# Performance work log

Hardware: AMD Instinct MI355X
Metric: run time of the kernel (lower is better)

Reference implementation:

```python
import jax, jax.numpy as jnp
import numpy as np

INPUT_SIZE = 9 * 7 * 32  # 2016
HIDDEN = 100
NUM_CLASSES = 3


def setup_inputs() -> dict:
    key = jax.random.key(0)
    ks = jax.random.split(key, 7)
    B, T = 256, 256
    s_ih = 1.0 / np.sqrt(HIDDEN)
    x = jax.random.normal(ks[0], (B, T, INPUT_SIZE), dtype=jnp.float32)
    # PyTorch LSTM params: gate order (i, f, g, o), each block of size HIDDEN
    W_ih = jax.random.uniform(ks[1], (4 * HIDDEN, INPUT_SIZE), jnp.float32, -s_ih, s_ih)
    W_hh = jax.random.uniform(ks[2], (4 * HIDDEN, HIDDEN), jnp.float32, -s_ih, s_ih)
    b_ih = jax.random.uniform(ks[3], (4 * HIDDEN,), jnp.float32, -s_ih, s_ih)
    b_hh = jax.random.uniform(ks[4], (4 * HIDDEN,), jnp.float32, -s_ih, s_ih)
    s_fc = 1.0 / np.sqrt(HIDDEN)
    W_fc = jax.random.uniform(ks[5], (NUM_CLASSES, HIDDEN), jnp.float32, -s_fc, s_fc)
    b_fc = jax.random.uniform(ks[6], (NUM_CLASSES,), jnp.float32, -s_fc, s_fc)
    return {"x": x, "W_ih": W_ih, "W_hh": W_hh, "b_ih": b_ih, "b_hh": b_hh,
            "W_fc": W_fc, "b_fc": b_fc}


def _lstm_last_hidden(x, W_ih, W_hh, b_ih, b_hh):
    B, T, _ = x.shape
    H = W_hh.shape[1]
    # Precompute input projection for all timesteps as one big GEMM: [B,T,4H]
    x_proj = jnp.einsum('bti,gi->btg', x, W_ih) + (b_ih + b_hh)
    x_proj = jnp.swapaxes(x_proj, 0, 1)  # [T, B, 4H] for scan over time

    def step(carry, xp_t):
        h, c = carry
        gates = xp_t + h @ W_hh.T  # [B, 4H]
        i, f, g, o = jnp.split(gates, 4, axis=-1)
        i = jax.nn.sigmoid(i)
        f = jax.nn.sigmoid(f)
        g = jnp.tanh(g)
        o = jax.nn.sigmoid(o)
        c = f * c + i * g
        h = o * jnp.tanh(c)
        return (h, c), None

    h0 = jnp.zeros((B, H), dtype=x.dtype)
    c0 = jnp.zeros((B, H), dtype=x.dtype)
    (hT, _), _ = jax.lax.scan(step, (h0, c0), x_proj)
    return hT  # [B, H] == out[:, -1, :]


def reference(x, W_ih, W_hh, b_ih, b_hh, W_fc, b_fc):
    hT = _lstm_last_hidden(x, W_ih, W_hh, b_ih, b_hh)
    return hT @ W_fc.T + b_fc  # [B, 3]
```

## Files before the change

### kernel.cpp

```cpp
#include <hip/hip_runtime.h>
#include <cstdint>
#include <cstddef>

#define DINL __device__ __forceinline__

typedef float f32x4 __attribute__((ext_vector_type(4)));
typedef unsigned short u16x8 __attribute__((ext_vector_type(8)));
typedef __bf16 bf16x8 __attribute__((ext_vector_type(8)));
typedef _Float16 half2v __attribute__((ext_vector_type(2)));

static constexpr int I_SZ  = 2016;
static constexpr int G4H   = 400;
static constexpr int HID   = 100;
static constexpr int BATCH = 256;
static constexpr int TLEN  = 256;
static constexpr int MROWS = BATCH * TLEN;
static constexpr int KT    = 63;
static constexpr int NPAD  = 512;
static constexpr int LD    = 40;

DINL unsigned short f2bf(float f) {
  unsigned u = __float_as_uint(f);
  u += 0x7fffu + ((u >> 16) & 1u);
  return (unsigned short)(u >> 16);
}
DINL float bf2f(unsigned short v) { return __uint_as_float(((unsigned)v) << 16); }

DINL void async16(const unsigned short* g, unsigned short* l) {
  __builtin_amdgcn_global_load_lds(
      (const __attribute__((address_space(1))) unsigned int*)g,
      (__attribute__((address_space(3))) unsigned int*)l, 16, 0, 0);
}

#if __has_builtin(__builtin_amdgcn_fdot2)
DINL float fdot2f(half2v a, half2v b, float c) { return __builtin_amdgcn_fdot2(a, b, c, false); }
#else
DINL float fdot2f(half2v a, half2v b, float c) {
  return c + (float)a[0] * (float)b[0] + (float)a[1] * (float)b[1];
}
#endif

#if __has_builtin(__builtin_amdgcn_exp2f)
DINL float ex2(float x) { return __builtin_amdgcn_exp2f(x); }
#else
DINL float ex2(float x) { return exp2f(x); }
#endif
#if __has_builtin(__builtin_amdgcn_rcpf)
DINL float rcpf_(float x) { return __builtin_amdgcn_rcpf(x); }
#else
DINL float rcpf_(float x) { return 1.0f / x; }
#endif

DINL float fast_sigmoid(float x) { return rcpf_(1.0f + ex2(-1.44269504f * x)); }
DINL float fast_tanh(float x)    { return 1.0f - 2.0f * rcpf_(1.0f + ex2(2.88539008f * x)); }

DINL half2v bch2(unsigned v) { return __builtin_bit_cast(half2v, v); }

__global__ void prep_kernel(const float* __restrict__ W_ih,
                            const float* __restrict__ b_ih,
                            const float* __restrict__ b_hh,
                            unsigned short* __restrict__ Wb,
                            float* __restrict__ biasb) {
  int idx = blockIdx.x * 256 + threadIdx.x;
  const int total = KT * NPAD * LD;
  if (idx < total) {
    int kt = idx / (NPAD * LD);
    int r  = idx - kt * (NPAD * LD);
    int n  = r / LD;
    int kk = r - n * LD;
    unsigned short v = 0;
    if (n < G4H && kk < 32) v = f2bf(W_ih[n * I_SZ + kt * 32 + kk]);
    Wb[idx] = v;
  }
  if (idx < NPAD) biasb[idx] = (idx < G4H) ? (b_ih[idx] + b_hh[idx]) : 0.0f;
}

__global__ __launch_bounds__(512) void gemm_xproj(
    const float* __restrict__ x, const unsigned short* __restrict__ Wb,
    const float* __restrict__ biasb, unsigned short* __restrict__ xp) {
  __shared__ unsigned short Ab[2][128 * LD];
  __shared__ unsigned short Bb[2][NPAD * LD];

  const int tid  = threadIdx.x;
  const int lane = tid & 63;
  const int wv   = tid >> 6;
  const int wm   = wv & 3;
  const int wn   = wv >> 2;
  const int m0   = blockIdx.x * 128;
  const int arow = tid >> 2;
  const int akq  = tid & 3;
  const int l15  = lane & 15;
  const int l4   = lane >> 4;

  f32x4 acc[2][13];
#pragma unroll
  for (int i = 0; i < 2; ++i)
#pragma unroll
    for (int j = 0; j < 13; ++j) acc[i][j] = (f32x4){0.f, 0.f, 0.f, 0.f};

  float4 a0, a1;
  const float* xr = x + (size_t)(m0 + arow) * I_SZ + akq * 8;

  auto loadA = [&](int kt) {
    const float* p = xr + kt * 32;
    a0 = *(const float4*)p;
    a1 = *(const float4*)(p + 4);
  };
  auto stageB = [&](int kt, int nb) {
    const unsigned short* src = Wb + (size_t)kt * (NPAD * LD) + lane * 8;
    unsigned short* dst = &Bb[nb][0];
#pragma unroll
    for (int i = 0; i < 5; ++i) {
      int c = wv + 8 * i;
      async16(src + c * 512, dst + c * 512);
    }
  };
  auto writeA = [&](int nb) {
    u16x8 u;
    u[0] = f2bf(a0.x); u[1] = f2bf(a0.y); u[2] = f2bf(a0.z); u[3] = f2bf(a0.w);
    u[4] = f2bf(a1.x); u[5] = f2bf(a1.y); u[6] = f2bf(a1.z); u[7] = f2bf(a1.w);
    *(u16x8*)&Ab[nb][arow * LD + akq * 8] = u;
  };

  loadA(0);
  stageB(0, 0);
  writeA(0);
  __syncthreads();

  int cur = 0;
  for (int kt = 0; kt < KT; ++kt) {
    if (kt < KT - 1) { loadA(kt + 1); stageB(kt + 1, cur ^ 1); }
    bf16x8 af0 = __builtin_bit_cast(bf16x8, *(const u16x8*)&Ab[cur][(wm * 32 + l15) * LD + l4 * 8]);
    bf16x8 af1 = __builtin_bit_cast(bf16x8, *(const u16x8*)&Ab[cur][(wm * 32 + 16 + l15) * LD + l4 * 8]);
#pragma unroll
    for (int nf = 0; nf < 13; ++nf) {
      bf16x8 bfr = __builtin_bit_cast(bf16x8,
          *(const u16x8*)&Bb[cur][(wn * 208 + nf * 16 + l15) * LD + l4 * 8]);
      acc[0][nf] = __builtin_amdgcn_mfma_f32_16x16x32_bf16(af0, bfr, acc[0][nf], 0, 0, 0);
      acc[1][nf] = __builtin_amdgcn_mfma_f32_16x16x32_bf16(af1, bfr, acc[1][nf], 0, 0, 0);
    }
    if (kt < KT - 1) writeA(cur ^ 1);
    __syncthreads();
    cur ^= 1;
  }

#pragma unroll
  for (int mf = 0; mf < 2; ++mf) {
#pragma unroll
    for (int nf = 0; nf < 13; ++nf) {
      int colf = wn * 208 + nf * 16;
      if (colf < G4H) {
        int col = colf + l15;
        float bias = biasb[col];
        int row = m0 + wm * 32 + mf * 16 + l4 * 4;
#pragma unroll
        for (int r = 0; r < 4; ++r)
          xp[(size_t)(row + r) * G4H + col] = f2bf(acc[mf][nf][r] + bias);
      }
    }
  }
}

__global__ __launch_bounds__(512) void lstm_rec(
    const unsigned short* __restrict__ xp, const float* __restrict__ W_hh,
    const float* __restrict__ W_fc, const float* __restrict__ b_fc,
    float* __restrict__ out) {
  __shared__ __align__(16) _Float16 h_lds[104];
  __shared__ float act[G4H];

  const int tid = threadIdx.x;
  const int b   = blockIdx.x;
  const int g   = tid;

  half2v w2[52];
  if (g < G4H) {
    const float* wr = W_hh + g * HID;
#pragma unroll
    for (int j = 0; j < 25; ++j) {
      float4 v = *(const float4*)(wr + 4 * j);
      w2[2 * j]     = (half2v){(_Float16)v.x, (_Float16)v.y};
      w2[2 * j + 1] = (half2v){(_Float16)v.z, (_Float16)v.w};
    }
    w2[50] = (half2v){(_Float16)0.f, (_Float16)0.f};
    w2[51] = (half2v){(_Float16)0.f, (_Float16)0.f};
  }
  if (tid < 104) h_lds[tid] = (_Float16)0.f;

  float c = 0.f, hreg = 0.f;
  unsigned short xpc = 0;
  if (g < G4H) xpc = xp[((size_t)b * TLEN + 0) * G4H + g];
  __syncthreads();

  for (int t = 0; t < TLEN; ++t) {
    unsigned short xpn = 0;
    if (t + 1 < TLEN && g < G4H)
      xpn = xp[((size_t)b * TLEN + t + 1) * G4H + g];

    if (g < G4H) {
      float s0 = bf2f(xpc), s1 = 0.f, s2 = 0.f, s3 = 0.f;
      const uint4* hv = (const uint4*)h_lds;
#pragma unroll
      for (int i = 0; i < 13; ++i) {
        uint4 u = hv[i];
        s0 = fdot2f(bch2(u.x), w2[4 * i + 0], s0);
        s1 = fdot2f(bch2(u.y), w2[4 * i + 1], s1);
        s2 = fdot2f(bch2(u.z), w2[4 * i + 2], s2);
        s3 = fdot2f(bch2(u.w), w2[4 * i + 3], s3);
      }
      float pre = (s0 + s1) + (s2 + s3);
      float a = (g < 200 || g >= 300) ? fast_sigmoid(pre) : fast_tanh(pre);
      act[g] = a;
    }
    __syncthreads();
    if (tid < HID) {
      float i_ = act[tid], f_ = act[tid + 100], g_ = act[tid + 200], o_ = act[tid + 300];
      c = f_ * c + i_ * g_;
      hreg = o_ * fast_tanh(c);
      h_lds[tid] = (_Float16)hreg;
    }
    __syncthreads();
    xpc = xpn;
  }

  if (tid < HID) act[tid] = hreg;
  __syncthreads();
  if (tid < 3) {
    float s = b_fc[tid];
    const float* wf = W_fc + tid * HID;
    for (int k = 0; k < HID; ++k) s += wf[k] * act[k];
    out[b * 3 + tid] = s;
  }
}

extern "C" void kernel_launch(void* const* d_in, const int* in_sizes, int n_in,
                              void* d_out, int out_size, void* d_ws, size_t ws_size,
                              hipStream_t stream) {
  const float* x    = (const float*)d_in[0];
  const float* W_ih = (const float*)d_in[1];
  const float* W_hh = (const float*)d_in[2];
  const float* b_ih = (const float*)d_in[3];
  const float* b_hh = (const float*)d_in[4];
  const float* W_fc = (const float*)d_in[5];
  const float* b_fc = (const float*)d_in[6];
  float* out = (float*)d_out;

  unsigned short* xp = (unsigned short*)d_ws;
  unsigned short* Wb = xp + (size_t)MROWS * G4H;
  float* biasb = (float*)(Wb + (size_t)KT * NPAD * LD);

  prep_kernel<<<(KT * NPAD * LD + 255) / 256, 256, 0, stream>>>(W_ih, b_ih, b_hh, Wb, biasb);
  gemm_xproj<<<MROWS / 128, 512, 0, stream>>>(x, Wb, biasb, xp);
  lstm_rec<<<BATCH, 512, 0, stream>>>(xp, W_hh, W_fc, b_fc, out);
}
```

Before: 1.045 ms.

## Retile GEMM warps to 64x112 and trim padded N columns

The input-projection GEMM now splits warps 2 along M and 4 along N, so each wave holds 4 A fragments and 6-7 B fragments instead of 2x13. This raises register reuse of B loads and cuts the padded N width from 512 to 416, which drops the wasted padding MFMA work and one async stage per k-tile. It also adds occupancy hints of 2 blocks per CU to the GEMM, and shrinks the recurrent kernel to 448 threads with the same hint. The larger accumulator tile raises register pressure, which may conflict with the occupancy target.

```diff
diff --git a/kernel.cpp b/kernel.cpp
--- a/kernel.cpp
+++ b/kernel.cpp
@@ -16,8 +16,9 @@
 static constexpr int TLEN  = 256;
 static constexpr int MROWS = BATCH * TLEN;
 static constexpr int KT    = 63;
-static constexpr int NPAD  = 512;
+static constexpr int NPADW = 416;
 static constexpr int LD    = 40;
+static constexpr int BSTG  = 16384;
 
 DINL unsigned short f2bf(float f) {
   unsigned u = __float_as_uint(f);
@@ -62,41 +63,44 @@
                             unsigned short* __restrict__ Wb,
                             float* __restrict__ biasb) {
   int idx = blockIdx.x * 256 + threadIdx.x;
-  const int total = KT * NPAD * LD;
+  const int total = KT * NPADW * LD;
   if (idx < total) {
-    int kt = idx / (NPAD * LD);
-    int r  = idx - kt * (NPAD * LD);
+    int kt = idx / (NPADW * LD);
+    int r  = idx - kt * (NPADW * LD);
     int n  = r / LD;
     int kk = r - n * LD;
     unsigned short v = 0;
     if (n < G4H && kk < 32) v = f2bf(W_ih[n * I_SZ + kt * 32 + kk]);
     Wb[idx] = v;
   }
-  if (idx < NPAD) biasb[idx] = (idx < G4H) ? (b_ih[idx] + b_hh[idx]) : 0.0f;
-}
-
-__global__ __launch_bounds__(512) void gemm_xproj(
+  if (idx < NPADW) biasb[idx] = (idx < G4H) ? (b_ih[idx] + b_hh[idx]) : 0.0f;
+}
+
+__global__ __launch_bounds__(512, 2) void gemm_xproj(
     const float* __restrict__ x, const unsigned short* __restrict__ Wb,
     const float* __restrict__ biasb, unsigned short* __restrict__ xp) {
-  __shared__ unsigned short Ab[2][128 * LD];
-  __shared__ unsigned short Bb[2][NPAD * LD];
+  __shared__ __align__(16) unsigned short Ab[2][128 * LD];
+  __shared__ __align__(16) unsigned short Bb[2][BSTG];
 
   const int tid  = threadIdx.x;
   const int lane = tid & 63;
   const int wv   = tid >> 6;
-  const int wm   = wv & 3;
-  const int wn   = wv >> 2;
+  const int wn   = wv & 3;
+  const int wm   = wv >> 2;
   const int m0   = blockIdx.x * 128;
   const int arow = tid >> 2;
   const int akq  = tid & 3;
   const int l15  = lane & 15;
   const int l4   = lane >> 4;
 
-  f32x4 acc[2][13];
-#pragma unroll
-  for (int i = 0; i < 2; ++i)
-#pragma unroll
-    for (int j = 0; j < 13; ++j) acc[i][j] = (f32x4){0.f, 0.f, 0.f, 0.f};
+  const int fst  = wn * 6 + (wn > 0);
+  const int fcnt = 7 - (wn > 0);
+
+  f32x4 acc[4][7];
+#pragma unroll
+  for (int i = 0; i < 4; ++i)
+#pragma unroll
+    for (int j = 0; j < 7; ++j) acc[i][j] = (f32x4){0.f, 0.f, 0.f, 0.f};
 
   float4 a0, a1;
   const float* xr = x + (size_t)(m0 + arow) * I_SZ + akq * 8;
@@ -107,10 +111,10 @@
     a1 = *(const float4*)(p + 4);
   };
   auto stageB = [&](int kt, int nb) {
-    const unsigned short* src = Wb + (size_t)kt * (NPAD * LD) + lane * 8;
+    const unsigned short* src = Wb + (size_t)kt * (NPADW * LD) + lane * 8;
     unsigned short* dst = &Bb[nb][0];
 #pragma unroll
-    for (int i = 0; i < 5; ++i) {
+    for (int i = 0; i < 4; ++i) {
       int c = wv + 8 * i;
       async16(src + c * 512, dst + c * 512);
     }
@@ -130,14 +134,20 @@
   int cur = 0;
   for (int kt = 0; kt < KT; ++kt) {
     if (kt < KT - 1) { loadA(kt + 1); stageB(kt + 1, cur ^ 1); }
-    bf16x8 af0 = __builtin_bit_cast(bf16x8, *(const u16x8*)&Ab[cur][(wm * 32 + l15) * LD + l4 * 8]);
-    bf16x8 af1 = __builtin_bit_cast(bf16x8, *(const u16x8*)&Ab[cur][(wm * 32 + 16 + l15) * LD + l4 * 8]);
-#pragma unroll
-    for (int nf = 0; nf < 13; ++nf) {
-      bf16x8 bfr = __builtin_bit_cast(bf16x8,
-          *(const u16x8*)&Bb[cur][(wn * 208 + nf * 16 + l15) * LD + l4 * 8]);
-      acc[0][nf] = __builtin_amdgcn_mfma_f32_16x16x32_bf16(af0, bfr, acc[0][nf], 0, 0, 0);
-      acc[1][nf] = __builtin_amdgcn_mfma_f32_16x16x32_bf16(af1, bfr, acc[1][nf], 0, 0, 0);
+    bf16x8 af[4];
+#pragma unroll
+    for (int mf = 0; mf < 4; ++mf)
+      af[mf] = __builtin_bit_cast(bf16x8,
+          *(const u16x8*)&Ab[cur][(wm * 64 + mf * 16 + l15) * LD + l4 * 8]);
+#pragma unroll
+    for (int j = 0; j < 7; ++j) {
+      if (j < fcnt) {
+        bf16x8 bfr = __builtin_bit_cast(bf16x8,
+            *(const u16x8*)&Bb[cur][((fst + j) * 16 + l15) * LD + l4 * 8]);
+#pragma unroll
+        for (int mf = 0; mf < 4; ++mf)
+          acc[mf][j] = __builtin_amdgcn_mfma_f32_16x16x32_bf16(af[mf], bfr, acc[mf][j], 0, 0, 0);
+      }
     }
     if (kt < KT - 1) writeA(cur ^ 1);
     __syncthreads();
@@ -145,23 +155,22 @@
   }
 
 #pragma unroll
-  for (int mf = 0; mf < 2; ++mf) {
-#pragma unroll
-    for (int nf = 0; nf < 13; ++nf) {
-      int colf = wn * 208 + nf * 16;
-      if (colf < G4H) {
-        int col = colf + l15;
+  for (int mf = 0; mf < 4; ++mf) {
+#pragma unroll
+    for (int j = 0; j < 7; ++j) {
+      if (j < fcnt) {
+        int col = (fst + j) * 16 + l15;
         float bias = biasb[col];
-        int row = m0 + wm * 32 + mf * 16 + l4 * 4;
+        int row = m0 + wm * 64 + mf * 16 + l4 * 4;
 #pragma unroll
         for (int r = 0; r < 4; ++r)
-          xp[(size_t)(row + r) * G4H + col] = f2bf(acc[mf][nf][r] + bias);
+          xp[(size_t)(row + r) * G4H + col] = f2bf(acc[mf][j][r] + bias);
       }
     }
   }
 }
 
-__global__ __launch_bounds__(512) void lstm_rec(
+__global__ __launch_bounds__(448, 2) void lstm_rec(
     const unsigned short* __restrict__ xp, const float* __restrict__ W_hh,
     const float* __restrict__ W_fc, const float* __restrict__ b_fc,
     float* __restrict__ out) {
@@ -188,13 +197,14 @@
 
   float c = 0.f, hreg = 0.f;
   unsigned short xpc = 0;
-  if (g < G4H) xpc = xp[((size_t)b * TLEN + 0) * G4H + g];
+  const unsigned short* xpb = xp + (size_t)b * TLEN * G4H;
+  if (g < G4H) xpc = xpb[g];
   __syncthreads();
 
   for (int t = 0; t < TLEN; ++t) {
     unsigned short xpn = 0;
     if (t + 1 < TLEN && g < G4H)
-      xpn = xp[((size_t)b * TLEN + t + 1) * G4H + g];
+      xpn = xpb[(t + 1) * G4H + g];
 
     if (g < G4H) {
       float s0 = bf2f(xpc), s1 = 0.f, s2 = 0.f, s3 = 0.f;
@@ -246,9 +256,9 @@
 
   unsigned short* xp = (unsigned short*)d_ws;
   unsigned short* Wb = xp + (size_t)MROWS * G4H;
-  float* biasb = (float*)(Wb + (size_t)KT * NPAD * LD);
-
-  prep_kernel<<<(KT * NPAD * LD + 255) / 256, 256, 0, stream>>>(W_ih, b_ih, b_hh, Wb, biasb);
+  float* biasb = (float*)(Wb + (size_t)KT * NPADW * LD);
+
+  prep_kernel<<<(KT * NPADW * LD + 255) / 256, 256, 0, stream>>>(W_ih, b_ih, b_hh, Wb, biasb);
   gemm_xproj<<<MROWS / 128, 512, 0, stream>>>(x, Wb, biasb, xp);
-  lstm_rec<<<BATCH, 512, 0, stream>>>(xp, W_hh, W_fc, b_fc, out);
-}
+  lstm_rec<<<BATCH, 448, 0, stream>>>(xp, W_hh, W_fc, b_fc, out);
+}
```

After: 1.028 ms. Within noise of the previous version (-1.6%).
